# Kernel optimization log

Measured on AMD Instinct MI355X. Metric: run time of the kernel, lower is better.

Reference implementation:

```python
import jax, jax.numpy as jnp
import numpy as np

N_NODES = 100000
N_EDGES = 1600000


def setup_inputs() -> dict:
    key = jax.random.key(0)
    ks = jax.random.split(key, 8)
    in_f, hid, out_c = 128, 128, 64
    return {
        "x": jax.random.normal(ks[0], (N_NODES, in_f), jnp.float32),
        "W_self1": jax.random.normal(ks[1], (in_f, hid), jnp.float32) * 0.05,
        "W_neigh1": jax.random.normal(ks[2], (in_f, hid), jnp.float32) * 0.05,
        "b1": jnp.zeros((hid,), jnp.float32),
        "W_self2": jax.random.normal(ks[3], (hid, out_c), jnp.float32) * 0.05,
        "W_neigh2": jax.random.normal(ks[4], (hid, out_c), jnp.float32) * 0.05,
        "b2": jnp.zeros((out_c,), jnp.float32),
        "src": jax.random.randint(ks[5], (N_EDGES,), 0, N_NODES, jnp.int32),
        "dst": jax.random.randint(ks[6], (N_EDGES,), 0, N_NODES, jnp.int32),
    }


def _sage_conv(h, src, dst, inv_deg, W_self, W_neigh, b):
    # mean aggregation over incoming neighbors: gather + segment-sum + normalize
    agg = jax.ops.segment_sum(h[src], dst, num_segments=N_NODES) * inv_deg  # [N, d]
    return h @ W_self + agg @ W_neigh + b


def reference(x, W_self1, W_neigh1, b1, W_self2, W_neigh2, b2, src, dst):
    # in-degree, clamped to 1 as in DGL SAGEConv
    deg = jax.ops.segment_sum(jnp.ones((N_EDGES,), x.dtype), dst, num_segments=N_NODES)
    inv_deg = (1.0 / jnp.maximum(deg, 1.0))[:, None]  # [N, 1]

    h1 = _sage_conv(x, src, dst, inv_deg, W_self1, W_neigh1, b1)      # conv1
    h1_relu = jax.nn.relu(h1)
    h2 = _sage_conv(h1_relu, src, dst, inv_deg, W_self2, W_neigh2, b2)  # conv2
    # original returns (h, middle_feat=[h1, relu(h1), h2])
    return (h2, h1, h1_relu, h2)
```

## Files before the change

kernel.cpp:

```cpp
#include <hip/hip_runtime.h>
#include <hip/hip_bf16.h>


#define NFEAT 128

typedef __bf16 bf16x8 __attribute__((ext_vector_type(8)));
typedef float  f32x4  __attribute__((ext_vector_type(4)));

static __device__ inline unsigned short f2bf(float f) {
    union { float f; unsigned int u; } v; v.f = f;
    unsigned int u = v.u;
    unsigned int r = (u + 0x7FFFu + ((u >> 16) & 1u)) >> 16;
    return (unsigned short)r;
}
static __device__ inline float bf2f(unsigned short h) {
    union { unsigned int u; float f; } v; v.u = ((unsigned int)h) << 16;
    return v.f;
}

__global__ __launch_bounds__(256) void k_deg(const int* __restrict__ dst,
                                             int* __restrict__ deg,
                                             int E, int P) {
    int part = blockIdx.x & 7;
    int slice = blockIdx.x >> 3;
    int nslices = gridDim.x >> 3;
    int per = (E + nslices - 1) / nslices;
    int beg = slice * per;
    int end = beg + per; if (end > E) end = E;
    int lo = part * P;
    int hi = lo + P;
    for (int e = beg + threadIdx.x; e < end; e += 256) {
        int d = dst[e];
        if (d >= lo && d < hi) atomicAdd(&deg[d], 1);
    }
}

__global__ __launch_bounds__(256) void k_scan1(const int* __restrict__ deg,
                                               int* __restrict__ escan,
                                               int* __restrict__ bsum, int n) {
    __shared__ int ws4[4];
    int tid = threadIdx.x;
    int base = blockIdx.x * 1024 + tid * 4;
    int d[4];
    #pragma unroll
    for (int j = 0; j < 4; ++j) d[j] = (base + j < n) ? deg[base + j] : 0;
    int s = d[0] + d[1] + d[2] + d[3];
    int lane = tid & 63, wid = tid >> 6;
    int incl = s;
    #pragma unroll
    for (int off = 1; off < 64; off <<= 1) {
        int t = __shfl_up(incl, off, 64);
        if (lane >= off) incl += t;
    }
    if (lane == 63) ws4[wid] = incl;
    __syncthreads();
    int wbase = 0;
    #pragma unroll
    for (int w = 0; w < 4; ++w) if (w < wid) wbase += ws4[w];
    int run = wbase + incl - s;
    #pragma unroll
    for (int j = 0; j < 4; ++j) {
        if (base + j < n) escan[base + j] = run;
        run += d[j];
    }
    if (tid == 255) bsum[blockIdx.x] = run;
}

__global__ __launch_bounds__(1024) void k_scan2(int* __restrict__ bsum, int nb) {
    __shared__ int ws16[16];
    int tid = threadIdx.x;
    int lane = tid & 63, wid = tid >> 6;
    int v = (tid < nb) ? bsum[tid] : 0;
    int incl = v;
    #pragma unroll
    for (int off = 1; off < 64; off <<= 1) {
        int t = __shfl_up(incl, off, 64);
        if (lane >= off) incl += t;
    }
    if (lane == 63) ws16[wid] = incl;
    __syncthreads();
    int wbase = 0;
    for (int w = 0; w < 16; ++w) if (w < wid) wbase += ws16[w];
    if (tid < nb) bsum[tid] = wbase + incl - v;
}

__global__ __launch_bounds__(256) void k_scan3(const int* __restrict__ deg,
                                               const int* __restrict__ escan,
                                               const int* __restrict__ bsum,
                                               int* __restrict__ offs,
                                               int* __restrict__ cursor,
                                               float* __restrict__ invd, int n) {
    int tid = threadIdx.x;
    int base = blockIdx.x * 1024 + tid * 4;
    int bb = bsum[blockIdx.x];
    #pragma unroll
    for (int j = 0; j < 4; ++j) {
        int i = base + j;
        if (i < n) {
            int d = deg[i];
            int off = escan[i] + bb;
            offs[i] = off;
            cursor[i] = off;
            invd[i] = 1.0f / fmaxf((float)d, 1.0f);
            if (i == n - 1) offs[n] = off + d;
        }
    }
}

__global__ __launch_bounds__(256) void k_cvt(const float* __restrict__ x,
                                             unsigned short* __restrict__ xb,
                                             int total4) {
    int i = blockIdx.x * 256 + threadIdx.x;
    if (i >= total4) return;
    float4 v = *(const float4*)(x + (size_t)i * 4);
    ushort4 o;
    o.x = f2bf(v.x); o.y = f2bf(v.y); o.z = f2bf(v.z); o.w = f2bf(v.w);
    *(ushort4*)(xb + (size_t)i * 4) = o;
}

__global__ __launch_bounds__(256) void k_wprep1(const float* __restrict__ Ws,
                                                const float* __restrict__ Wn,
                                                unsigned short* __restrict__ wb) {
    int idx = blockIdx.x * 256 + threadIdx.x;
    if (idx >= 32768) return;
    int j = idx & 7, lane = (idx >> 3) & 63, ct = (idx >> 9) & 7, ks = idx >> 12;
    int k = ks * 32 + ((lane >> 4) & 3) * 8 + j;
    int n = ct * 16 + (lane & 15);
    float v = (k < 128) ? Ws[k * 128 + n] : Wn[(k - 128) * 128 + n];
    wb[idx] = f2bf(v);
}

__global__ __launch_bounds__(256) void k_wprep2(const float* __restrict__ Ws,
                                                const float* __restrict__ Wn,
                                                unsigned short* __restrict__ wb) {
    int idx = blockIdx.x * 256 + threadIdx.x;
    if (idx >= 16384) return;
    int j = idx & 7, lane = (idx >> 3) & 63, ct = (idx >> 9) & 7, ks = idx >> 12;
    int k = ks * 32 + ((lane >> 4) & 3) * 8 + j;
    int n = ct * 16 + (lane & 15);
    float v = (n < 64) ? Ws[k * 64 + n] : Wn[k * 64 + (n - 64)];
    wb[idx] = f2bf(v);
}

__global__ __launch_bounds__(256) void k_scatter(const int* __restrict__ src,
                                                 const int* __restrict__ dst,
                                                 int* __restrict__ cursor,
                                                 int* __restrict__ ssrc,
                                                 int E, int P) {
    int part = blockIdx.x & 7;
    int slice = blockIdx.x >> 3;
    int nslices = gridDim.x >> 3;
    int per = (E + nslices - 1) / nslices;
    int beg = slice * per;
    int end = beg + per; if (end > E) end = E;
    int lo = part * P;
    int hi = lo + P;
    for (int e = beg + threadIdx.x; e < end; e += 256) {
        int d = dst[e];
        if (d >= lo && d < hi) {
            int pos = atomicAdd(&cursor[d], 1);
            ssrc[pos] = src[e];
        }
    }
}

__global__ __launch_bounds__(256) void k_agg1(const unsigned short* __restrict__ xb,
                                              const int* __restrict__ offs,
                                              const int* __restrict__ ssrc,
                                              const float* __restrict__ invd,
                                              unsigned short* __restrict__ aggb,
                                              int n) {
    int node = blockIdx.x * 8 + (threadIdx.x >> 5);
    if (node >= n) return;
    int lane = threadIdx.x & 31;
    int beg = offs[node], end = offs[node + 1];
    float p0 = 0.f, p1 = 0.f, p2 = 0.f, p3 = 0.f;
    float q0 = 0.f, q1 = 0.f, q2 = 0.f, q3 = 0.f;
    float r0 = 0.f, r1 = 0.f, r2 = 0.f, r3 = 0.f;
    float t0 = 0.f, t1 = 0.f, t2 = 0.f, t3 = 0.f;
    int e = beg;
    for (; e + 8 <= end; e += 8) {
        int s0 = ssrc[e + 0], s1 = ssrc[e + 1], s2 = ssrc[e + 2], s3 = ssrc[e + 3];
        int s4 = ssrc[e + 4], s5 = ssrc[e + 5], s6 = ssrc[e + 6], s7 = ssrc[e + 7];
        ushort4 v0 = *(const ushort4*)(xb + (size_t)s0 * NFEAT + lane * 4);
        ushort4 v1 = *(const ushort4*)(xb + (size_t)s1 * NFEAT + lane * 4);
        ushort4 v2 = *(const ushort4*)(xb + (size_t)s2 * NFEAT + lane * 4);
        ushort4 v3 = *(const ushort4*)(xb + (size_t)s3 * NFEAT + lane * 4);
        ushort4 v4 = *(const ushort4*)(xb + (size_t)s4 * NFEAT + lane * 4);
        ushort4 v5 = *(const ushort4*)(xb + (size_t)s5 * NFEAT + lane * 4);
        ushort4 v6 = *(const ushort4*)(xb + (size_t)s6 * NFEAT + lane * 4);
        ushort4 v7 = *(const ushort4*)(xb + (size_t)s7 * NFEAT + lane * 4);
        p0 += bf2f(v0.x); p1 += bf2f(v0.y); p2 += bf2f(v0.z); p3 += bf2f(v0.w);
        q0 += bf2f(v1.x); q1 += bf2f(v1.y); q2 += bf2f(v1.z); q3 += bf2f(v1.w);
        r0 += bf2f(v2.x); r1 += bf2f(v2.y); r2 += bf2f(v2.z); r3 += bf2f(v2.w);
        t0 += bf2f(v3.x); t1 += bf2f(v3.y); t2 += bf2f(v3.z); t3 += bf2f(v3.w);
        p0 += bf2f(v4.x); p1 += bf2f(v4.y); p2 += bf2f(v4.z); p3 += bf2f(v4.w);
        q0 += bf2f(v5.x); q1 += bf2f(v5.y); q2 += bf2f(v5.z); q3 += bf2f(v5.w);
        r0 += bf2f(v6.x); r1 += bf2f(v6.y); r2 += bf2f(v6.z); r3 += bf2f(v6.w);
        t0 += bf2f(v7.x); t1 += bf2f(v7.y); t2 += bf2f(v7.z); t3 += bf2f(v7.w);
    }
    for (; e + 4 <= end; e += 4) {
        int s0 = ssrc[e + 0], s1 = ssrc[e + 1], s2 = ssrc[e + 2], s3 = ssrc[e + 3];
        ushort4 v0 = *(const ushort4*)(xb + (size_t)s0 * NFEAT + lane * 4);
        ushort4 v1 = *(const ushort4*)(xb + (size_t)s1 * NFEAT + lane * 4);
        ushort4 v2 = *(const ushort4*)(xb + (size_t)s2 * NFEAT + lane * 4);
        ushort4 v3 = *(const ushort4*)(xb + (size_t)s3 * NFEAT + lane * 4);
        p0 += bf2f(v0.x); p1 += bf2f(v0.y); p2 += bf2f(v0.z); p3 += bf2f(v0.w);
        q0 += bf2f(v1.x); q1 += bf2f(v1.y); q2 += bf2f(v1.z); q3 += bf2f(v1.w);
        r0 += bf2f(v2.x); r1 += bf2f(v2.y); r2 += bf2f(v2.z); r3 += bf2f(v2.w);
        t0 += bf2f(v3.x); t1 += bf2f(v3.y); t2 += bf2f(v3.z); t3 += bf2f(v3.w);
    }
    for (; e < end; ++e) {
        int s = ssrc[e];
        ushort4 v = *(const ushort4*)(xb + (size_t)s * NFEAT + lane * 4);
        p0 += bf2f(v.x); p1 += bf2f(v.y); p2 += bf2f(v.z); p3 += bf2f(v.w);
    }
    float a0 = (p0 + q0) + (r0 + t0);
    float a1 = (p1 + q1) + (r1 + t1);
    float a2 = (p2 + q2) + (r2 + t2);
    float a3 = (p3 + q3) + (r3 + t3);
    float iv = invd[node];
    ushort4 o;
    o.x = f2bf(a0 * iv); o.y = f2bf(a1 * iv);
    o.z = f2bf(a2 * iv); o.w = f2bf(a3 * iv);
    *(ushort4*)(aggb + (size_t)node * NFEAT + lane * 4) = o;
}

__global__ __launch_bounds__(256) void k_mm1(const unsigned short* __restrict__ xb,
                                             const unsigned short* __restrict__ aggb,
                                             const unsigned short* __restrict__ wb,
                                             const float* __restrict__ bias,
                                             float* __restrict__ h1,
                                             float* __restrict__ h1r,
                                             unsigned short* __restrict__ h1rb,
                                             int M) {
    int wave = threadIdx.x >> 6, lane = threadIdx.x & 63;
    int rowbase = blockIdx.x * 64 + wave * 16;
    f32x4 acc[8];
    #pragma unroll
    for (int ct = 0; ct < 8; ++ct) acc[ct] = (f32x4){0.f, 0.f, 0.f, 0.f};

    int arow = rowbase + (lane & 15);
    if (arow >= M) arow = M - 1;
    int kq = ((lane >> 4) & 3) * 8;

    #pragma unroll 1
    for (int ks = 0; ks < 8; ++ks) {
        const unsigned short* Ap = (ks < 4) ? xb : aggb;
        bf16x8 a = *(const bf16x8*)(Ap + (size_t)arow * 128 + (ks & 3) * 32 + kq);
        const unsigned short* wp = wb + ((size_t)ks * 8 * 64 + lane) * 8;
        #pragma unroll
        for (int ct = 0; ct < 8; ++ct) {
            bf16x8 b = *(const bf16x8*)(wp + (size_t)ct * 512);
            acc[ct] = __builtin_amdgcn_mfma_f32_16x16x32_bf16(a, b, acc[ct], 0, 0, 0);
        }
    }

    int r0 = rowbase + ((lane >> 4) & 3) * 4;
    int col0 = lane & 15;
    #pragma unroll
    for (int ct = 0; ct < 8; ++ct) {
        int col = ct * 16 + col0;
        float bv = bias[col];
        #pragma unroll
        for (int i = 0; i < 4; ++i) {
            int row = r0 + i;
            if (row < M) {
                float v = acc[ct][i] + bv;
                float vr = fmaxf(v, 0.f);
                size_t o = (size_t)row * 128 + col;
                h1[o] = v;
                h1r[o] = vr;
                h1rb[o] = f2bf(vr);
            }
        }
    }
}

__global__ __launch_bounds__(256) void k_mm2(const unsigned short* __restrict__ h1rb,
                                             const unsigned short* __restrict__ wb,
                                             float* __restrict__ s2,
                                             unsigned short* __restrict__ p2b,
                                             int M) {
    int wave = threadIdx.x >> 6, lane = threadIdx.x & 63;
    int rowbase = blockIdx.x * 64 + wave * 16;
    f32x4 acc[8];
    #pragma unroll
    for (int ct = 0; ct < 8; ++ct) acc[ct] = (f32x4){0.f, 0.f, 0.f, 0.f};

    int arow = rowbase + (lane & 15);
    if (arow >= M) arow = M - 1;
    int kq = ((lane >> 4) & 3) * 8;

    #pragma unroll 1
    for (int ks = 0; ks < 4; ++ks) {
        bf16x8 a = *(const bf16x8*)(h1rb + (size_t)arow * 128 + ks * 32 + kq);
        const unsigned short* wp = wb + ((size_t)ks * 8 * 64 + lane) * 8;
        #pragma unroll
        for (int ct = 0; ct < 8; ++ct) {
            bf16x8 b = *(const bf16x8*)(wp + (size_t)ct * 512);
            acc[ct] = __builtin_amdgcn_mfma_f32_16x16x32_bf16(a, b, acc[ct], 0, 0, 0);
        }
    }

    int r0 = rowbase + ((lane >> 4) & 3) * 4;
    int col0 = lane & 15;
    #pragma unroll
    for (int ct = 0; ct < 8; ++ct) {
        int col = ct * 16 + col0;
        #pragma unroll
        for (int i = 0; i < 4; ++i) {
            int row = r0 + i;
            if (row < M) {
                float v = acc[ct][i];
                if (col < 64)
                    s2[(size_t)row * 64 + col] = v;
                else
                    p2b[(size_t)row * 64 + (col - 64)] = f2bf(v);
            }
        }
    }
}

__global__ __launch_bounds__(256) void k_agg2(const unsigned short* __restrict__ p2b,
                                              const int* __restrict__ offs,
                                              const int* __restrict__ ssrc,
                                              const float* __restrict__ invd,
                                              const float* __restrict__ s2,
                                              const float* __restrict__ b2,
                                              float* __restrict__ h2a,
                                              float* __restrict__ h2b, int n) {
    int node = blockIdx.x * 16 + (threadIdx.x >> 4);
    if (node >= n) return;
    int lane = threadIdx.x & 15;
    int beg = offs[node], end = offs[node + 1];
    float p0 = 0.f, p1 = 0.f, p2 = 0.f, p3 = 0.f;
    float q0 = 0.f, q1 = 0.f, q2 = 0.f, q3 = 0.f;
    float r0 = 0.f, r1 = 0.f, r2 = 0.f, r3 = 0.f;
    float t0 = 0.f, t1 = 0.f, t2 = 0.f, t3 = 0.f;
    int e = beg;
    for (; e + 8 <= end; e += 8) {
        int s0 = ssrc[e + 0], s1 = ssrc[e + 1], s2i = ssrc[e + 2], s3 = ssrc[e + 3];
        int s4 = ssrc[e + 4], s5 = ssrc[e + 5], s6 = ssrc[e + 6], s7 = ssrc[e + 7];
        ushort4 v0 = *(const ushort4*)(p2b + (size_t)s0 * 64 + lane * 4);
        ushort4 v1 = *(const ushort4*)(p2b + (size_t)s1 * 64 + lane * 4);
        ushort4 v2 = *(const ushort4*)(p2b + (size_t)s2i * 64 + lane * 4);
        ushort4 v3 = *(const ushort4*)(p2b + (size_t)s3 * 64 + lane * 4);
        ushort4 v4 = *(const ushort4*)(p2b + (size_t)s4 * 64 + lane * 4);
        ushort4 v5 = *(const ushort4*)(p2b + (size_t)s5 * 64 + lane * 4);
        ushort4 v6 = *(const ushort4*)(p2b + (size_t)s6 * 64 + lane * 4);
        ushort4 v7 = *(const ushort4*)(p2b + (size_t)s7 * 64 + lane * 4);
        p0 += bf2f(v0.x); p1 += bf2f(v0.y); p2 += bf2f(v0.z); p3 += bf2f(v0.w);
        q0 += bf2f(v1.x); q1 += bf2f(v1.y); q2 += bf2f(v1.z); q3 += bf2f(v1.w);
        r0 += bf2f(v2.x); r1 += bf2f(v2.y); r2 += bf2f(v2.z); r3 += bf2f(v2.w);
        t0 += bf2f(v3.x); t1 += bf2f(v3.y); t2 += bf2f(v3.z); t3 += bf2f(v3.w);
        p0 += bf2f(v4.x); p1 += bf2f(v4.y); p2 += bf2f(v4.z); p3 += bf2f(v4.w);
        q0 += bf2f(v5.x); q1 += bf2f(v5.y); q2 += bf2f(v5.z); q3 += bf2f(v5.w);
        r0 += bf2f(v6.x); r1 += bf2f(v6.y); r2 += bf2f(v6.z); r3 += bf2f(v6.w);
        t0 += bf2f(v7.x); t1 += bf2f(v7.y); t2 += bf2f(v7.z); t3 += bf2f(v7.w);
    }
    for (; e + 4 <= end; e += 4) {
        int s0 = ssrc[e + 0], s1 = ssrc[e + 1], s2i = ssrc[e + 2], s3 = ssrc[e + 3];
        ushort4 v0 = *(const ushort4*)(p2b + (size_t)s0 * 64 + lane * 4);
        ushort4 v1 = *(const ushort4*)(p2b + (size_t)s1 * 64 + lane * 4);
        ushort4 v2 = *(const ushort4*)(p2b + (size_t)s2i * 64 + lane * 4);
        ushort4 v3 = *(const ushort4*)(p2b + (size_t)s3 * 64 + lane * 4);
        p0 += bf2f(v0.x); p1 += bf2f(v0.y); p2 += bf2f(v0.z); p3 += bf2f(v0.w);
        q0 += bf2f(v1.x); q1 += bf2f(v1.y); q2 += bf2f(v1.z); q3 += bf2f(v1.w);
        r0 += bf2f(v2.x); r1 += bf2f(v2.y); r2 += bf2f(v2.z); r3 += bf2f(v2.w);
        t0 += bf2f(v3.x); t1 += bf2f(v3.y); t2 += bf2f(v3.z); t3 += bf2f(v3.w);
    }
    for (; e < end; ++e) {
        int s = ssrc[e];
        ushort4 v = *(const ushort4*)(p2b + (size_t)s * 64 + lane * 4);
        p0 += bf2f(v.x); p1 += bf2f(v.y); p2 += bf2f(v.z); p3 += bf2f(v.w);
    }
    float a0 = (p0 + q0) + (r0 + t0);
    float a1 = (p1 + q1) + (r1 + t1);
    float a2 = (p2 + q2) + (r2 + t2);
    float a3 = (p3 + q3) + (r3 + t3);
    float iv = invd[node];
    float4 sv = *(const float4*)(s2 + (size_t)node * 64 + lane * 4);
    float4 bv = *(const float4*)(b2 + lane * 4);
    float4 r = make_float4(sv.x + a0 * iv + bv.x, sv.y + a1 * iv + bv.y,
                           sv.z + a2 * iv + bv.z, sv.w + a3 * iv + bv.w);
    *(float4*)(h2a + (size_t)node * 64 + lane * 4) = r;
    *(float4*)(h2b + (size_t)node * 64 + lane * 4) = r;
}

static inline size_t align256(size_t x) { return (x + 255) & ~(size_t)255; }

extern "C" void kernel_launch(void* const* d_in, const int* in_sizes, int n_in,
                              void* d_out, int out_size, void* d_ws, size_t ws_size,
                              hipStream_t stream) {
    const float* x   = (const float*)d_in[0];
    const float* Ws1 = (const float*)d_in[1];
    const float* Wn1 = (const float*)d_in[2];
    const float* b1  = (const float*)d_in[3];
    const float* Ws2 = (const float*)d_in[4];
    const float* Wn2 = (const float*)d_in[5];
    const float* b2  = (const float*)d_in[6];
    const int* src   = (const int*)d_in[7];
    const int* dst   = (const int*)d_in[8];

    int E = in_sizes[7];
    int N = in_sizes[0] / NFEAT;

    float* out = (float*)d_out;
    float* h2a = out;
    float* h1  = out + (size_t)N * 64;
    float* h1r = out + (size_t)N * 192;
    float* h2b = out + (size_t)N * 320;

    char* ws = (char*)d_ws;
    size_t off = 0;
    int*   deg    = (int*)(ws + off);  off = align256(off + (size_t)4 * N);
    int*   offs   = (int*)(ws + off);  off = align256(off + (size_t)4 * (N + 1));
    int*   cursor = (int*)(ws + off);  off = align256(off + (size_t)4 * N);
    float* invd   = (float*)(ws + off); off = align256(off + (size_t)4 * N);
    int*   escan  = (int*)(ws + off);  off = align256(off + (size_t)4 * N);
    int*   bsum   = (int*)(ws + off);  off = align256(off + (size_t)4 * 1024);
    int*   ssrc   = (int*)(ws + off);  off = align256(off + (size_t)4 * E);
    unsigned short* wb1 = (unsigned short*)(ws + off); off = align256(off + 2 * 32768);
    unsigned short* wb2 = (unsigned short*)(ws + off); off = align256(off + 2 * 16384);
    unsigned short* xb = (unsigned short*)(ws + off);
    float*          s2 = (float*)(ws + off);
    off = align256(off + (size_t)N * NFEAT * 2);
    unsigned short* aggb = (unsigned short*)(ws + off);
    unsigned short* p2b  = (unsigned short*)(ws + off);
    off = align256(off + (size_t)N * NFEAT * 2);
    unsigned short* h1rb = (unsigned short*)(ws + off);
    off += (size_t)N * NFEAT * 2;

    int nb = (N + 1023) / 1024;
    int P = (N + 7) / 8;

    hipMemsetAsync(deg, 0, (size_t)4 * N, stream);
    k_deg<<<8 * 256, 256, 0, stream>>>(dst, deg, E, P);
    k_scan1<<<nb, 256, 0, stream>>>(deg, escan, bsum, N);
    k_scan2<<<1, 1024, 0, stream>>>(bsum, nb);
    k_scan3<<<nb, 256, 0, stream>>>(deg, escan, bsum, offs, cursor, invd, N);
    k_cvt<<<(N * 32 + 255) / 256, 256, 0, stream>>>(x, xb, N * 32);
    k_wprep1<<<128, 256, 0, stream>>>(Ws1, Wn1, wb1);
    k_wprep2<<<64, 256, 0, stream>>>(Ws2, Wn2, wb2);
    k_scatter<<<8 * 256, 256, 0, stream>>>(src, dst, cursor, ssrc, E, P);

    k_agg1<<<(N + 7) / 8, 256, 0, stream>>>(xb, offs, ssrc, invd, aggb, N);
    k_mm1<<<(N + 63) / 64, 256, 0, stream>>>(xb, aggb, wb1, b1, h1, h1r, h1rb, N);
    k_mm2<<<(N + 63) / 64, 256, 0, stream>>>(h1rb, wb2, s2, p2b, N);
    k_agg2<<<(N + 15) / 16, 256, 0, stream>>>(p2b, offs, ssrc, invd, s2, b2, h2a, h2b, N);
}
```

Baseline: 543.0 us.

## Fuse layer-1 neighbor aggregation into the MFMA GEMM and merge prep kernels

Layer-1 mean aggregation now runs inside the GEMM kernel. Each lane gathers neighbor rows directly in the MFMA A-fragment layout and feeds them as bf16 operands, so the aggb intermediate buffer and its write/read round trip are gone. The x-conversion and the two weight-prep kernels are merged into one launch, and the output stores become nontemporal. The risk is that the gather, where each lane reads four 16-byte chunks per neighbor row and the unroll is only 2, may be less coalesced and less latency-tolerant than the old 32-lane-per-node aggregation. It also adds register pressure inside the MFMA kernel.

```diff
diff --git a/kernel.cpp b/kernel.cpp
--- a/kernel.cpp
+++ b/kernel.cpp
@@ -6,6 +6,7 @@
 
 typedef __bf16 bf16x8 __attribute__((ext_vector_type(8)));
 typedef float  f32x4  __attribute__((ext_vector_type(4)));
+typedef unsigned short ushort8v __attribute__((ext_vector_type(8)));
 
 static __device__ inline unsigned short f2bf(float f) {
     union { float f; unsigned int u; } v; v.f = f;
@@ -107,39 +108,38 @@
     }
 }
 
-__global__ __launch_bounds__(256) void k_cvt(const float* __restrict__ x,
-                                             unsigned short* __restrict__ xb,
-                                             int total4) {
-    int i = blockIdx.x * 256 + threadIdx.x;
-    if (i >= total4) return;
-    float4 v = *(const float4*)(x + (size_t)i * 4);
-    ushort4 o;
-    o.x = f2bf(v.x); o.y = f2bf(v.y); o.z = f2bf(v.z); o.w = f2bf(v.w);
-    *(ushort4*)(xb + (size_t)i * 4) = o;
-}
-
-__global__ __launch_bounds__(256) void k_wprep1(const float* __restrict__ Ws,
-                                                const float* __restrict__ Wn,
-                                                unsigned short* __restrict__ wb) {
-    int idx = blockIdx.x * 256 + threadIdx.x;
-    if (idx >= 32768) return;
-    int j = idx & 7, lane = (idx >> 3) & 63, ct = (idx >> 9) & 7, ks = idx >> 12;
-    int k = ks * 32 + ((lane >> 4) & 3) * 8 + j;
-    int n = ct * 16 + (lane & 15);
-    float v = (k < 128) ? Ws[k * 128 + n] : Wn[(k - 128) * 128 + n];
-    wb[idx] = f2bf(v);
-}
-
-__global__ __launch_bounds__(256) void k_wprep2(const float* __restrict__ Ws,
-                                                const float* __restrict__ Wn,
-                                                unsigned short* __restrict__ wb) {
-    int idx = blockIdx.x * 256 + threadIdx.x;
-    if (idx >= 16384) return;
-    int j = idx & 7, lane = (idx >> 3) & 63, ct = (idx >> 9) & 7, ks = idx >> 12;
-    int k = ks * 32 + ((lane >> 4) & 3) * 8 + j;
-    int n = ct * 16 + (lane & 15);
-    float v = (n < 64) ? Ws[k * 64 + n] : Wn[k * 64 + (n - 64)];
-    wb[idx] = f2bf(v);
+__global__ __launch_bounds__(256) void k_prep(const float* __restrict__ x,
+                                              unsigned short* __restrict__ xb,
+                                              const float* __restrict__ Ws1,
+                                              const float* __restrict__ Wn1,
+                                              unsigned short* __restrict__ wb1,
+                                              const float* __restrict__ Ws2,
+                                              const float* __restrict__ Wn2,
+                                              unsigned short* __restrict__ wb2,
+                                              int total4, int C) {
+    int b = blockIdx.x;
+    if (b < C) {
+        int i = b * 256 + threadIdx.x;
+        if (i >= total4) return;
+        float4 v = *(const float4*)(x + (size_t)i * 4);
+        ushort4 o;
+        o.x = f2bf(v.x); o.y = f2bf(v.y); o.z = f2bf(v.z); o.w = f2bf(v.w);
+        *(ushort4*)(xb + (size_t)i * 4) = o;
+    } else if (b < C + 128) {
+        int idx = (b - C) * 256 + threadIdx.x;
+        int j = idx & 7, lane = (idx >> 3) & 63, ct = (idx >> 9) & 7, ks = idx >> 12;
+        int k = ks * 32 + ((lane >> 4) & 3) * 8 + j;
+        int n = ct * 16 + (lane & 15);
+        float v = (k < 128) ? Ws1[k * 128 + n] : Wn1[(k - 128) * 128 + n];
+        wb1[idx] = f2bf(v);
+    } else {
+        int idx = (b - C - 128) * 256 + threadIdx.x;
+        int j = idx & 7, lane = (idx >> 3) & 63, ct = (idx >> 9) & 7, ks = idx >> 12;
+        int k = ks * 32 + ((lane >> 4) & 3) * 8 + j;
+        int n = ct * 16 + (lane & 15);
+        float v = (n < 64) ? Ws2[k * 64 + n] : Wn2[k * 64 + (n - 64)];
+        wb2[idx] = f2bf(v);
+    }
 }
 
 __global__ __launch_bounds__(256) void k_scatter(const int* __restrict__ src,
@@ -164,99 +164,110 @@
     }
 }
 
-__global__ __launch_bounds__(256) void k_agg1(const unsigned short* __restrict__ xb,
+__global__ __launch_bounds__(256) void k_mm1f(const unsigned short* __restrict__ xb,
                                               const int* __restrict__ offs,
                                               const int* __restrict__ ssrc,
                                               const float* __restrict__ invd,
-                                              unsigned short* __restrict__ aggb,
-                                              int n) {
-    int node = blockIdx.x * 8 + (threadIdx.x >> 5);
-    if (node >= n) return;
-    int lane = threadIdx.x & 31;
-    int beg = offs[node], end = offs[node + 1];
-    float p0 = 0.f, p1 = 0.f, p2 = 0.f, p3 = 0.f;
-    float q0 = 0.f, q1 = 0.f, q2 = 0.f, q3 = 0.f;
-    float r0 = 0.f, r1 = 0.f, r2 = 0.f, r3 = 0.f;
-    float t0 = 0.f, t1 = 0.f, t2 = 0.f, t3 = 0.f;
-    int e = beg;
-    for (; e + 8 <= end; e += 8) {
-        int s0 = ssrc[e + 0], s1 = ssrc[e + 1], s2 = ssrc[e + 2], s3 = ssrc[e + 3];
-        int s4 = ssrc[e + 4], s5 = ssrc[e + 5], s6 = ssrc[e + 6], s7 = ssrc[e + 7];
-        ushort4 v0 = *(const ushort4*)(xb + (size_t)s0 * NFEAT + lane * 4);
-        ushort4 v1 = *(const ushort4*)(xb + (size_t)s1 * NFEAT + lane * 4);
-        ushort4 v2 = *(const ushort4*)(xb + (size_t)s2 * NFEAT + lane * 4);
-        ushort4 v3 = *(const ushort4*)(xb + (size_t)s3 * NFEAT + lane * 4);
-        ushort4 v4 = *(const ushort4*)(xb + (size_t)s4 * NFEAT + lane * 4);
-        ushort4 v5 = *(const ushort4*)(xb + (size_t)s5 * NFEAT + lane * 4);
-        ushort4 v6 = *(const ushort4*)(xb + (size_t)s6 * NFEAT + lane * 4);
-        ushort4 v7 = *(const ushort4*)(xb + (size_t)s7 * NFEAT + lane * 4);
-        p0 += bf2f(v0.x); p1 += bf2f(v0.y); p2 += bf2f(v0.z); p3 += bf2f(v0.w);
-        q0 += bf2f(v1.x); q1 += bf2f(v1.y); q2 += bf2f(v1.z); q3 += bf2f(v1.w);
-        r0 += bf2f(v2.x); r1 += bf2f(v2.y); r2 += bf2f(v2.z); r3 += bf2f(v2.w);
-        t0 += bf2f(v3.x); t1 += bf2f(v3.y); t2 += bf2f(v3.z); t3 += bf2f(v3.w);
-        p0 += bf2f(v4.x); p1 += bf2f(v4.y); p2 += bf2f(v4.z); p3 += bf2f(v4.w);
-        q0 += bf2f(v5.x); q1 += bf2f(v5.y); q2 += bf2f(v5.z); q3 += bf2f(v5.w);
-        r0 += bf2f(v6.x); r1 += bf2f(v6.y); r2 += bf2f(v6.z); r3 += bf2f(v6.w);
-        t0 += bf2f(v7.x); t1 += bf2f(v7.y); t2 += bf2f(v7.z); t3 += bf2f(v7.w);
-    }
-    for (; e + 4 <= end; e += 4) {
-        int s0 = ssrc[e + 0], s1 = ssrc[e + 1], s2 = ssrc[e + 2], s3 = ssrc[e + 3];
-        ushort4 v0 = *(const ushort4*)(xb + (size_t)s0 * NFEAT + lane * 4);
-        ushort4 v1 = *(const ushort4*)(xb + (size_t)s1 * NFEAT + lane * 4);
-        ushort4 v2 = *(const ushort4*)(xb + (size_t)s2 * NFEAT + lane * 4);
-        ushort4 v3 = *(const ushort4*)(xb + (size_t)s3 * NFEAT + lane * 4);
-        p0 += bf2f(v0.x); p1 += bf2f(v0.y); p2 += bf2f(v0.z); p3 += bf2f(v0.w);
-        q0 += bf2f(v1.x); q1 += bf2f(v1.y); q2 += bf2f(v1.z); q3 += bf2f(v1.w);
-        r0 += bf2f(v2.x); r1 += bf2f(v2.y); r2 += bf2f(v2.z); r3 += bf2f(v2.w);
-        t0 += bf2f(v3.x); t1 += bf2f(v3.y); t2 += bf2f(v3.z); t3 += bf2f(v3.w);
-    }
-    for (; e < end; ++e) {
-        int s = ssrc[e];
-        ushort4 v = *(const ushort4*)(xb + (size_t)s * NFEAT + lane * 4);
-        p0 += bf2f(v.x); p1 += bf2f(v.y); p2 += bf2f(v.z); p3 += bf2f(v.w);
-    }
-    float a0 = (p0 + q0) + (r0 + t0);
-    float a1 = (p1 + q1) + (r1 + t1);
-    float a2 = (p2 + q2) + (r2 + t2);
-    float a3 = (p3 + q3) + (r3 + t3);
-    float iv = invd[node];
-    ushort4 o;
-    o.x = f2bf(a0 * iv); o.y = f2bf(a1 * iv);
-    o.z = f2bf(a2 * iv); o.w = f2bf(a3 * iv);
-    *(ushort4*)(aggb + (size_t)node * NFEAT + lane * 4) = o;
-}
-
-__global__ __launch_bounds__(256) void k_mm1(const unsigned short* __restrict__ xb,
-                                             const unsigned short* __restrict__ aggb,
-                                             const unsigned short* __restrict__ wb,
-                                             const float* __restrict__ bias,
-                                             float* __restrict__ h1,
-                                             float* __restrict__ h1r,
-                                             unsigned short* __restrict__ h1rb,
-                                             int M) {
+                                              const unsigned short* __restrict__ wb,
+                                              const float* __restrict__ bias,
+                                              float* __restrict__ h1,
+                                              float* __restrict__ h1r,
+                                              unsigned short* __restrict__ h1rb,
+                                              int M) {
     int wave = threadIdx.x >> 6, lane = threadIdx.x & 63;
     int rowbase = blockIdx.x * 64 + wave * 16;
+    int node = rowbase + (lane & 15);
+    if (node >= M) node = M - 1;
+    int q = (lane >> 4) & 3;
+    int kq = q * 8;
+
+    float a0[8], a1[8], a2[8], a3[8];
+    #pragma unroll
+    for (int jj = 0; jj < 8; ++jj) { a0[jj]=0.f; a1[jj]=0.f; a2[jj]=0.f; a3[jj]=0.f; }
+    int beg = offs[node], end = offs[node + 1];
+    int e = beg;
+    for (; e + 2 <= end; e += 2) {
+        int s0 = ssrc[e], s1 = ssrc[e + 1];
+        const unsigned short* r0p = xb + (size_t)s0 * NFEAT + kq;
+        const unsigned short* r1p = xb + (size_t)s1 * NFEAT + kq;
+        ushort8v u0 = *(const ushort8v*)(r0p);
+        ushort8v u1 = *(const ushort8v*)(r0p + 32);
+        ushort8v u2 = *(const ushort8v*)(r0p + 64);
+        ushort8v u3 = *(const ushort8v*)(r0p + 96);
+        ushort8v w0 = *(const ushort8v*)(r1p);
+        ushort8v w1 = *(const ushort8v*)(r1p + 32);
+        ushort8v w2 = *(const ushort8v*)(r1p + 64);
+        ushort8v w3 = *(const ushort8v*)(r1p + 96);
+        #pragma unroll
+        for (int jj = 0; jj < 8; ++jj) {
+            a0[jj] += bf2f(u0[jj]) + bf2f(w0[jj]);
+            a1[jj] += bf2f(u1[jj]) + bf2f(w1[jj]);
+            a2[jj] += bf2f(u2[jj]) + bf2f(w2[jj]);
+            a3[jj] += bf2f(u3[jj]) + bf2f(w3[jj]);
+        }
+    }
+    if (e < end) {
+        int s0 = ssrc[e];
+        const unsigned short* rp = xb + (size_t)s0 * NFEAT + kq;
+        ushort8v u0 = *(const ushort8v*)(rp);
+        ushort8v u1 = *(const ushort8v*)(rp + 32);
+        ushort8v u2 = *(const ushort8v*)(rp + 64);
+        ushort8v u3 = *(const ushort8v*)(rp + 96);
+        #pragma unroll
+        for (int jj = 0; jj < 8; ++jj) {
+            a0[jj] += bf2f(u0[jj]);
+            a1[jj] += bf2f(u1[jj]);
+            a2[jj] += bf2f(u2[jj]);
+            a3[jj] += bf2f(u3[jj]);
+        }
+    }
+    float iv = invd[node];
+    ushort8v g0, g1, g2, g3;
+    #pragma unroll
+    for (int jj = 0; jj < 8; ++jj) {
+        g0[jj] = f2bf(a0[jj] * iv); g1[jj] = f2bf(a1[jj] * iv);
+        g2[jj] = f2bf(a2[jj] * iv); g3[jj] = f2bf(a3[jj] * iv);
+    }
+    bf16x8 ag0 = *(bf16x8*)&g0;
+    bf16x8 ag1 = *(bf16x8*)&g1;
+    bf16x8 ag2 = *(bf16x8*)&g2;
+    bf16x8 ag3 = *(bf16x8*)&g3;
+
     f32x4 acc[8];
     #pragma unroll
     for (int ct = 0; ct < 8; ++ct) acc[ct] = (f32x4){0.f, 0.f, 0.f, 0.f};
 
-    int arow = rowbase + (lane & 15);
-    if (arow >= M) arow = M - 1;
-    int kq = ((lane >> 4) & 3) * 8;
-
     #pragma unroll 1
-    for (int ks = 0; ks < 8; ++ks) {
-        const unsigned short* Ap = (ks < 4) ? xb : aggb;
-        bf16x8 a = *(const bf16x8*)(Ap + (size_t)arow * 128 + (ks & 3) * 32 + kq);
-        const unsigned short* wp = wb + ((size_t)ks * 8 * 64 + lane) * 8;
+    for (int ks = 0; ks < 4; ++ks) {
+        bf16x8 a = *(const bf16x8*)(xb + (size_t)node * NFEAT + ks * 32 + kq);
+        const unsigned short* wp = wb + ((size_t)ks * 512 + lane) * 8;
         #pragma unroll
         for (int ct = 0; ct < 8; ++ct) {
             bf16x8 b = *(const bf16x8*)(wp + (size_t)ct * 512);
             acc[ct] = __builtin_amdgcn_mfma_f32_16x16x32_bf16(a, b, acc[ct], 0, 0, 0);
         }
     }
-
-    int r0 = rowbase + ((lane >> 4) & 3) * 4;
+    {
+        const unsigned short* wl = wb + (size_t)lane * 8;
+        #pragma unroll
+        for (int ct = 0; ct < 8; ++ct)
+            acc[ct] = __builtin_amdgcn_mfma_f32_16x16x32_bf16(
+                ag0, *(const bf16x8*)(wl + (size_t)4 * 4096 + ct * 512), acc[ct], 0, 0, 0);
+        #pragma unroll
+        for (int ct = 0; ct < 8; ++ct)
+            acc[ct] = __builtin_amdgcn_mfma_f32_16x16x32_bf16(
+                ag1, *(const bf16x8*)(wl + (size_t)5 * 4096 + ct * 512), acc[ct], 0, 0, 0);
+        #pragma unroll
+        for (int ct = 0; ct < 8; ++ct)
+            acc[ct] = __builtin_amdgcn_mfma_f32_16x16x32_bf16(
+                ag2, *(const bf16x8*)(wl + (size_t)6 * 4096 + ct * 512), acc[ct], 0, 0, 0);
+        #pragma unroll
+        for (int ct = 0; ct < 8; ++ct)
+            acc[ct] = __builtin_amdgcn_mfma_f32_16x16x32_bf16(
+                ag3, *(const bf16x8*)(wl + (size_t)7 * 4096 + ct * 512), acc[ct], 0, 0, 0);
+    }
+
+    int r0 = rowbase + q * 4;
     int col0 = lane & 15;
     #pragma unroll
     for (int ct = 0; ct < 8; ++ct) {
@@ -269,8 +280,8 @@
                 float v = acc[ct][i] + bv;
                 float vr = fmaxf(v, 0.f);
                 size_t o = (size_t)row * 128 + col;
-                h1[o] = v;
-                h1r[o] = vr;
+                __builtin_nontemporal_store(v, &h1[o]);
+                __builtin_nontemporal_store(vr, &h1r[o]);
                 h1rb[o] = f2bf(vr);
             }
         }
@@ -295,7 +306,7 @@
     #pragma unroll 1
     for (int ks = 0; ks < 4; ++ks) {
         bf16x8 a = *(const bf16x8*)(h1rb + (size_t)arow * 128 + ks * 32 + kq);
-        const unsigned short* wp = wb + ((size_t)ks * 8 * 64 + lane) * 8;
+        const unsigned short* wp = wb + ((size_t)ks * 512 + lane) * 8;
         #pragma unroll
         for (int ct = 0; ct < 8; ++ct) {
             bf16x8 b = *(const bf16x8*)(wp + (size_t)ct * 512);
@@ -382,10 +393,13 @@
     float iv = invd[node];
     float4 sv = *(const float4*)(s2 + (size_t)node * 64 + lane * 4);
     float4 bv = *(const float4*)(b2 + lane * 4);
-    float4 r = make_float4(sv.x + a0 * iv + bv.x, sv.y + a1 * iv + bv.y,
-                           sv.z + a2 * iv + bv.z, sv.w + a3 * iv + bv.w);
-    *(float4*)(h2a + (size_t)node * 64 + lane * 4) = r;
-    *(float4*)(h2b + (size_t)node * 64 + lane * 4) = r;
+    f32x4 r;
+    r[0] = sv.x + a0 * iv + bv.x;
+    r[1] = sv.y + a1 * iv + bv.y;
+    r[2] = sv.z + a2 * iv + bv.z;
+    r[3] = sv.w + a3 * iv + bv.w;
+    __builtin_nontemporal_store(r, (f32x4*)(h2a + (size_t)node * 64 + lane * 4));
+    __builtin_nontemporal_store(r, (f32x4*)(h2b + (size_t)node * 64 + lane * 4));
 }
 
 static inline size_t align256(size_t x) { return (x + 255) & ~(size_t)255; }
@@ -426,27 +440,26 @@
     unsigned short* xb = (unsigned short*)(ws + off);
     float*          s2 = (float*)(ws + off);
     off = align256(off + (size_t)N * NFEAT * 2);
-    unsigned short* aggb = (unsigned short*)(ws + off);
-    unsigned short* p2b  = (unsigned short*)(ws + off);
-    off = align256(off + (size_t)N * NFEAT * 2);
+    unsigned short* p2b = (unsigned short*)(ws + off);
+    off = align256(off + (size_t)N * 64 * 2);
     unsigned short* h1rb = (unsigned short*)(ws + off);
     off += (size_t)N * NFEAT * 2;
 
     int nb = (N + 1023) / 1024;
     int P = (N + 7) / 8;
+    int C = (N * 32 + 255) / 256;
 
     hipMemsetAsync(deg, 0, (size_t)4 * N, stream);
     k_deg<<<8 * 256, 256, 0, stream>>>(dst, deg, E, P);
     k_scan1<<<nb, 256, 0, stream>>>(deg, escan, bsum, N);
     k_scan2<<<1, 1024, 0, stream>>>(bsum, nb);
     k_scan3<<<nb, 256, 0, stream>>>(deg, escan, bsum, offs, cursor, invd, N);
-    k_cvt<<<(N * 32 + 255) / 256, 256, 0, stream>>>(x, xb, N * 32);
-    k_wprep1<<<128, 256, 0, stream>>>(Ws1, Wn1, wb1);
-    k_wprep2<<<64, 256, 0, stream>>>(Ws2, Wn2, wb2);
+    k_prep<<<C + 192, 256, 0, stream>>>(x, xb, Ws1, Wn1, wb1, Ws2, Wn2, wb2,
+                                        N * 32, C);
     k_scatter<<<8 * 256, 256, 0, stream>>>(src, dst, cursor, ssrc, E, P);
 
-    k_agg1<<<(N + 7) / 8, 256, 0, stream>>>(xb, offs, ssrc, invd, aggb, N);
-    k_mm1<<<(N + 63) / 64, 256, 0, stream>>>(xb, aggb, wb1, b1, h1, h1r, h1rb, N);
+    k_mm1f<<<(N + 63) / 64, 256, 0, stream>>>(xb, offs, ssrc, invd, wb1, b1,
+                                              h1, h1r, h1rb, N);
     k_mm2<<<(N + 63) / 64, 256, 0, stream>>>(h1rb, wb2, s2, p2b, N);
     k_agg2<<<(N + 15) / 16, 256, 0, stream>>>(p2b, offs, ssrc, invd, s2, b2, h2a, h2b, N);
 }
```

Result: faster. 515.9 us (-5.0%).
